# Performance work log

Hardware: AMD Instinct MI355X
Metric: run time of the kernel (lower is better)

The kernel has to match this reference:

```python
import jax, jax.numpy as jnp
import numpy as np

N1, N2, C = 1024, 1024, 128
H = 2 * C  # h_dim = in_dim * 2


def setup_inputs() -> dict:
    key = jax.random.key(0)
    ks = jax.random.split(key, 8)
    std = 0.01
    return {
        "X": jax.random.normal(ks[0], (N1, C), dtype=jnp.float32),
        "Y": jax.random.normal(ks[1], (N2, C), dtype=jnp.float32),
        "Wsr": jax.random.normal(ks[2], (C, C), dtype=jnp.float32) * std,
        "Wtg": jax.random.normal(ks[3], (C, C), dtype=jnp.float32) * std,
        "W1": jax.random.normal(ks[4], (H, H), dtype=jnp.float32) * std,
        "b1": jnp.zeros((H,), dtype=jnp.float32),
        "W2": jax.random.normal(ks[5], (1, H), dtype=jnp.float32) * std,
        "b2": jnp.zeros((1,), dtype=jnp.float32),
    }


def reference(X, Y, Wsr, Wtg, W1, b1, W2, b2):
    # project_sr / project_tg (bias-free Linear: x @ W^T)
    Xp = X @ Wsr.T  # [N1, C]
    Yp = Y @ Wtg.T  # [N2, C]
    # First fc_M linear on concat([X_k, Y_k]) == split-weight form:
    # concat(x, y) @ W1^T = x @ W1[:, :C]^T + y @ W1[:, C:]^T
    Xh = Xp @ W1[:, :C].T  # [N1, 2C]
    Yh = Yp @ W1[:, C:].T  # [N2, 2C]
    Hid = jax.nn.relu(Xh[:, None, :] + Yh[None, :, :] + b1)  # [N1, N2, 2C]
    # Second linear 2C -> 1, then squeeze
    M = jnp.einsum('abh,h->ab', Hid, W2[0]) + b2[0]  # [N1, N2]
    return M
```

## Files before the change

kernel.cpp:

```cpp
#include <hip/hip_runtime.h>

#define N1 1024
#define N2 1024
#define CDIM 128
#define HDIM 256


__global__ __launch_bounds__(256) void fold_weights(
    const float* __restrict__ W1, const float* __restrict__ Wsr,
    const float* __restrict__ Wtg, float* __restrict__ Wx,
    float* __restrict__ Wy) {
  int id = blockIdx.x * 256 + threadIdx.x;
  int m  = id / (HDIM * CDIM);
  int r  = id % (HDIM * CDIM);
  int h  = r / CDIM;
  int j  = r % CDIM;
  const float* Wm    = m ? Wtg : Wsr;
  const float* w1row = W1 + (size_t)h * HDIM + (m ? CDIM : 0);
  float acc = 0.f;
#pragma unroll 8
  for (int c = 0; c < CDIM; ++c)
    acc = fmaf(w1row[c], Wm[(size_t)c * CDIM + j], acc);
  (m ? Wy : Wx)[(size_t)h * CDIM + j] = acc;
}

__global__ __launch_bounds__(256) void gemm_ht(
    const float* __restrict__ X, const float* __restrict__ Y,
    const float* __restrict__ Wx, const float* __restrict__ Wy,
    const float* __restrict__ b1, float* __restrict__ XhT,
    float* __restrict__ YhT) {
  const float* A = blockIdx.z ? Y : X;
  const float* W = blockIdx.z ? Wy : Wx;
  float*       O = blockIdx.z ? YhT : XhT;
  const bool useBias = (blockIdx.z == 0);

  __shared__ float Al[64][132];
  __shared__ float Wl[128][68];

  const int t  = threadIdx.x;
  const int n0 = blockIdx.x * 64;
  const int h0 = blockIdx.y * 64;

#pragma unroll
  for (int it = 0; it < 8; ++it) {
    int row = it * 8 + (t >> 5);
    int col = (t & 31) * 4;
    *(float4*)(&Al[row][col]) =
        *(const float4*)(&A[(size_t)(n0 + row) * CDIM + col]);
  }
#pragma unroll
  for (int it = 0; it < 8; ++it) {
    int h = it * 8 + (t >> 5);
    int k = (t & 31) * 4;
    float4 w = *(const float4*)(&W[(size_t)(h0 + h) * CDIM + k]);
    Wl[k + 0][h] = w.x;
    Wl[k + 1][h] = w.y;
    Wl[k + 2][h] = w.z;
    Wl[k + 3][h] = w.w;
  }
  __syncthreads();

  const int tx = t & 15;
  const int ty = t >> 4;
  float acc[4][4];
#pragma unroll
  for (int i = 0; i < 4; ++i)
#pragma unroll
    for (int j = 0; j < 4; ++j) acc[i][j] = 0.f;

  for (int k4 = 0; k4 < CDIM; k4 += 4) {
    float a_[4][4];
#pragma unroll
    for (int i = 0; i < 4; ++i) {
      float4 v = *(const float4*)(&Al[ty * 4 + i][k4]);
      a_[i][0] = v.x; a_[i][1] = v.y; a_[i][2] = v.z; a_[i][3] = v.w;
    }
#pragma unroll
    for (int kk = 0; kk < 4; ++kk) {
      float4 w = *(const float4*)(&Wl[k4 + kk][tx * 4]);
      float wj[4] = {w.x, w.y, w.z, w.w};
#pragma unroll
      for (int i = 0; i < 4; ++i)
#pragma unroll
        for (int j = 0; j < 4; ++j)
          acc[i][j] = fmaf(a_[i][kk], wj[j], acc[i][j]);
    }
  }

#pragma unroll
  for (int j = 0; j < 4; ++j) {
    int h = h0 + tx * 4 + j;
    float b = useBias ? b1[h] : 0.f;
    float4 v = {acc[0][j] + b, acc[1][j] + b, acc[2][j] + b, acc[3][j] + b};
    *(float4*)(&O[(size_t)h * N1 + n0 + ty * 4]) = v;
  }
}

__global__ __launch_bounds__(256, 2) void pairwise_part(
    const float* __restrict__ XhT, const float* __restrict__ YhT,
    const float* __restrict__ W2, float* __restrict__ Pbase) {
  __shared__ float Xl[64][64];
  __shared__ float Yl[64][128];

  const int t  = threadIdx.x;
  const int b0 = blockIdx.x * 128;
  const int a0 = blockIdx.y * 64;
  const int hb = blockIdx.z * 64;
  float* P = Pbase + (size_t)blockIdx.z * ((size_t)N1 * N2);

#pragma unroll
  for (int it = 0; it < 4; ++it) {
    int idx = it * 256 + t;
    int hl  = idx >> 4;
    int c4  = (idx & 15) * 4;
    *(float4*)(&Xl[hl][c4]) =
        *(const float4*)(&XhT[(size_t)(hb + hl) * N1 + a0 + c4]);
  }
#pragma unroll
  for (int it = 0; it < 8; ++it) {
    int idx = it * 256 + t;
    int hl  = idx >> 5;
    int c   = idx & 31;
    int pos = (c >> 1) | ((c & 1) << 4);
    *(float4*)(&Yl[hl][pos * 4]) =
        *(const float4*)(&YhT[(size_t)(hb + hl) * N2 + b0 + c * 4]);
  }
  __syncthreads();

  const int tx = t & 15;
  const int ty = t >> 4;

  float acc[4][8];
#pragma unroll
  for (int i = 0; i < 4; ++i)
#pragma unroll
    for (int j = 0; j < 8; ++j) acc[i][j] = 0.f;

  for (int h4 = 0; h4 < 64; h4 += 4) {
    const float4 w4 = *(const float4*)(&W2[hb + h4]);
    const float wh[4] = {w4.x, w4.y, w4.z, w4.w};
#pragma unroll
    for (int hh = 0; hh < 4; ++hh) {
      const int h = h4 + hh;
      float4 xv = *(const float4*)(&Xl[h][ty * 4]);
      float4 yv0 = *(const float4*)(&Yl[h][tx * 4]);
      float4 yv1 = *(const float4*)(&Yl[h][64 + tx * 4]);
      const float xa[4] = {xv.x, xv.y, xv.z, xv.w};
      const float yb[8] = {yv0.x, yv0.y, yv0.z, yv0.w,
                           yv1.x, yv1.y, yv1.z, yv1.w};
      const float w = wh[hh];
#pragma unroll
      for (int i = 0; i < 4; ++i) {
#pragma unroll
        for (int j = 0; j < 8; j += 2) {
          float s0 = xa[i] + yb[j];
          float s1 = xa[i] + yb[j + 1];
          float r0 = fmaxf(s0, 0.f);
          float r1 = fmaxf(s1, 0.f);
          acc[i][j]     = fmaf(r0, w, acc[i][j]);
          acc[i][j + 1] = fmaf(r1, w, acc[i][j + 1]);
        }
      }
    }
  }

#pragma unroll
  for (int i = 0; i < 4; ++i) {
    int a = a0 + ty * 4 + i;
    float4 v0 = {acc[i][0], acc[i][1], acc[i][2], acc[i][3]};
    float4 v1 = {acc[i][4], acc[i][5], acc[i][6], acc[i][7]};
    *(float4*)(&P[(size_t)a * N2 + b0 + tx * 8])     = v0;
    *(float4*)(&P[(size_t)a * N2 + b0 + tx * 8 + 4]) = v1;
  }
}

__global__ __launch_bounds__(256) void finalize(
    const float* __restrict__ P0, const float* __restrict__ P1,
    const float* __restrict__ P2, const float* __restrict__ P3,
    const float* __restrict__ b2, float* __restrict__ out) {
  int i4 = blockIdx.x * 256 + threadIdx.x;
  float4 a = ((const float4*)P0)[i4];
  float4 b = ((const float4*)P1)[i4];
  float4 c = ((const float4*)P2)[i4];
  float4 d = ((const float4*)P3)[i4];
  const float bb = b2[0];
  float4 o = {a.x + b.x + c.x + d.x + bb, a.y + b.y + c.y + d.y + bb,
              a.z + b.z + c.z + d.z + bb, a.w + b.w + c.w + d.w + bb};
  ((float4*)out)[i4] = o;
}

extern "C" void kernel_launch(void* const* d_in, const int* in_sizes, int n_in,
                              void* d_out, int out_size, void* d_ws,
                              size_t ws_size, hipStream_t stream) {
  const float* X   = (const float*)d_in[0];
  const float* Y   = (const float*)d_in[1];
  const float* Wsr = (const float*)d_in[2];
  const float* Wtg = (const float*)d_in[3];
  const float* W1  = (const float*)d_in[4];
  const float* b1  = (const float*)d_in[5];
  const float* W2  = (const float*)d_in[6];
  const float* b2  = (const float*)d_in[7];
  float* out = (float*)d_out;

  float* ws  = (float*)d_ws;
  float* Wx  = ws;
  float* Wy  = ws + 32768;
  float* XhT = ws + 65536;
  float* YhT = ws + 65536 + 262144;
  float* P   = ws + 589824;

  fold_weights<<<256, 256, 0, stream>>>(W1, Wsr, Wtg, Wx, Wy);
  gemm_ht<<<dim3(16, 4, 2), 256, 0, stream>>>(X, Y, Wx, Wy, b1, XhT, YhT);
  pairwise_part<<<dim3(8, 16, 4), 256, 0, stream>>>(XhT, YhT, W2, P);
  finalize<<<1024, 256, 0, stream>>>(P, P + 1048576, P + 2097152,
                                     P + 3145728, b2, out);
}
```

Before: 114.9 us.

## Rewrite ReLU as half-sum plus abs to drop the max from the pairwise loop

Uses relu(s) = 0.5*(s + |s|). The linear parts, 0.5*W2·Xh and 0.5*W2·Yh, are computed once per row and column in a new small reduction kernel. The pairwise loop now only accumulates |x+y|*w, where the abs can fold into the fma as an input modifier, so one VALU op per element is removed. The hidden-dim split also changes from 4×64 to 8×32 with a higher occupancy hint. The trade-off is that partial-sum writes and finalize reads double in memory traffic, and finalize must add the broadcast row and column terms.

```diff
diff --git a/kernel.cpp b/kernel.cpp
--- a/kernel.cpp
+++ b/kernel.cpp
@@ -96,20 +96,33 @@
   }
 }
 
-__global__ __launch_bounds__(256, 2) void pairwise_part(
+__global__ __launch_bounds__(256) void uv_reduce(
+    const float* __restrict__ XhT, const float* __restrict__ YhT,
+    const float* __restrict__ W2, float* __restrict__ uv) {
+  int tid = blockIdx.x * 256 + threadIdx.x;
+  const float* T = (tid < N1) ? XhT : YhT;
+  int n = tid & (N1 - 1);
+  float acc = 0.f;
+#pragma unroll 8
+  for (int h = 0; h < HDIM; ++h)
+    acc = fmaf(T[(size_t)h * N1 + n], W2[h], acc);
+  uv[tid] = 0.5f * acc;
+}
+
+__global__ __launch_bounds__(256, 4) void pairwise_abs(
     const float* __restrict__ XhT, const float* __restrict__ YhT,
     const float* __restrict__ W2, float* __restrict__ Pbase) {
-  __shared__ float Xl[64][64];
-  __shared__ float Yl[64][128];
+  __shared__ float Xl[32][64];
+  __shared__ float Yl[32][128];
 
   const int t  = threadIdx.x;
   const int b0 = blockIdx.x * 128;
   const int a0 = blockIdx.y * 64;
-  const int hb = blockIdx.z * 64;
+  const int hb = blockIdx.z * 32;
   float* P = Pbase + (size_t)blockIdx.z * ((size_t)N1 * N2);
 
 #pragma unroll
-  for (int it = 0; it < 4; ++it) {
+  for (int it = 0; it < 2; ++it) {
     int idx = it * 256 + t;
     int hl  = idx >> 4;
     int c4  = (idx & 15) * 4;
@@ -117,7 +130,7 @@
         *(const float4*)(&XhT[(size_t)(hb + hl) * N1 + a0 + c4]);
   }
 #pragma unroll
-  for (int it = 0; it < 8; ++it) {
+  for (int it = 0; it < 4; ++it) {
     int idx = it * 256 + t;
     int hl  = idx >> 5;
     int c   = idx & 31;
@@ -136,13 +149,13 @@
 #pragma unroll
     for (int j = 0; j < 8; ++j) acc[i][j] = 0.f;
 
-  for (int h4 = 0; h4 < 64; h4 += 4) {
+  for (int h4 = 0; h4 < 32; h4 += 4) {
     const float4 w4 = *(const float4*)(&W2[hb + h4]);
-    const float wh[4] = {w4.x, w4.y, w4.z, w4.w};
+    const float wh[4] = {0.5f * w4.x, 0.5f * w4.y, 0.5f * w4.z, 0.5f * w4.w};
 #pragma unroll
     for (int hh = 0; hh < 4; ++hh) {
       const int h = h4 + hh;
-      float4 xv = *(const float4*)(&Xl[h][ty * 4]);
+      float4 xv  = *(const float4*)(&Xl[h][ty * 4]);
       float4 yv0 = *(const float4*)(&Yl[h][tx * 4]);
       float4 yv1 = *(const float4*)(&Yl[h][64 + tx * 4]);
       const float xa[4] = {xv.x, xv.y, xv.z, xv.w};
@@ -155,10 +168,8 @@
         for (int j = 0; j < 8; j += 2) {
           float s0 = xa[i] + yb[j];
           float s1 = xa[i] + yb[j + 1];
-          float r0 = fmaxf(s0, 0.f);
-          float r1 = fmaxf(s1, 0.f);
-          acc[i][j]     = fmaf(r0, w, acc[i][j]);
-          acc[i][j + 1] = fmaf(r1, w, acc[i][j + 1]);
+          acc[i][j]     = fmaf(__builtin_fabsf(s0), w, acc[i][j]);
+          acc[i][j + 1] = fmaf(__builtin_fabsf(s1), w, acc[i][j + 1]);
         }
       }
     }
@@ -175,17 +186,21 @@
 }
 
 __global__ __launch_bounds__(256) void finalize(
-    const float* __restrict__ P0, const float* __restrict__ P1,
-    const float* __restrict__ P2, const float* __restrict__ P3,
+    const float* __restrict__ P, const float* __restrict__ uv,
     const float* __restrict__ b2, float* __restrict__ out) {
   int i4 = blockIdx.x * 256 + threadIdx.x;
-  float4 a = ((const float4*)P0)[i4];
-  float4 b = ((const float4*)P1)[i4];
-  float4 c = ((const float4*)P2)[i4];
-  float4 d = ((const float4*)P3)[i4];
-  const float bb = b2[0];
-  float4 o = {a.x + b.x + c.x + d.x + bb, a.y + b.y + c.y + d.y + bb,
-              a.z + b.z + c.z + d.z + bb, a.w + b.w + c.w + d.w + bb};
+  int a  = i4 >> 8;
+  int c4 = i4 & 255;
+  float4 s = ((const float4*)P)[i4];
+#pragma unroll
+  for (int z = 1; z < 8; ++z) {
+    float4 p = ((const float4*)(P + (size_t)z * N1 * N2))[i4];
+    s.x += p.x; s.y += p.y; s.z += p.z; s.w += p.w;
+  }
+  const float ua = uv[a] + b2[0];
+  float4 vb = ((const float4*)(uv + N1))[c4];
+  float4 o = {s.x + ua + vb.x, s.y + ua + vb.y, s.z + ua + vb.z,
+              s.w + ua + vb.w};
   ((float4*)out)[i4] = o;
 }
 
@@ -207,11 +222,12 @@
   float* Wy  = ws + 32768;
   float* XhT = ws + 65536;
   float* YhT = ws + 65536 + 262144;
-  float* P   = ws + 589824;
+  float* uv  = ws + 589824;
+  float* P   = ws + 591872;
 
   fold_weights<<<256, 256, 0, stream>>>(W1, Wsr, Wtg, Wx, Wy);
   gemm_ht<<<dim3(16, 4, 2), 256, 0, stream>>>(X, Y, Wx, Wy, b1, XhT, YhT);
-  pairwise_part<<<dim3(8, 16, 4), 256, 0, stream>>>(XhT, YhT, W2, P);
-  finalize<<<1024, 256, 0, stream>>>(P, P + 1048576, P + 2097152,
-                                     P + 3145728, b2, out);
-}
+  uv_reduce<<<8, 256, 0, stream>>>(XhT, YhT, W2, uv);
+  pairwise_abs<<<dim3(8, 16, 8), 256, 0, stream>>>(XhT, YhT, W2, P);
+  finalize<<<1024, 256, 0, stream>>>(P, uv, b2, out);
+}
```

Result: slower. 135.2 us (+17.7%).
